# Performance work log

Measured on AMD Instinct MI355X. Metric: run time of the kernel, lower is better.

The kernel has to match this reference:

```python
import jax, jax.numpy as jnp
import numpy as np

B, S, D = 4, 1024, 1024
H = 16
DH = D // H  # head dim = 64
SCALE = DH ** -0.5
NEG = -1e18


def setup_inputs() -> dict:
    key = jax.random.key(0)
    ks = jax.random.split(key, 8)
    queries = jax.random.normal(ks[0], (B, S, D), dtype=jnp.float32)
    keys_ = jax.random.normal(ks[1], (B, S, D), dtype=jnp.float32)
    values = jax.random.normal(ks[2], (B, S, D), dtype=jnp.float32)
    mask = jax.random.randint(ks[3], (B, 1, S), 0, 2).astype(bool)
    sd = 1.0 / np.sqrt(D)
    Wq = jax.random.normal(ks[4], (D, D), dtype=jnp.float32) * sd
    Wk = jax.random.normal(ks[5], (D, D), dtype=jnp.float32) * sd
    Wv = jax.random.normal(ks[6], (D, D), dtype=jnp.float32) * sd
    Wo = jax.random.normal(ks[7], (D, D), dtype=jnp.float32) * sd
    return {"queries": queries, "keys": keys_, "values": values,
            "Wq": Wq, "Wk": Wk, "Wv": Wv, "Wo": Wo, "mask": mask}


def _split_heads(x):
    # [B,S,D] -> [B,H,S,DH]
    b, s, d = x.shape
    return x.reshape(b, s, H, d // H).transpose(0, 2, 1, 3)


def reference(queries, keys, values, Wq, Wk, Wv, Wo, mask):
    q = _split_heads(queries @ Wq) * SCALE          # [B,H,S,DH]
    k = _split_heads(keys @ Wk)                     # [B,H,S,DH]
    v = _split_heads(values @ Wv)                   # [B,H,S,DH]
    logits = jnp.einsum('bhqd,bhkd->bhqk', q, k)    # [B,H,S,S]
    # mask [B,1,Lk] -> unsqueeze head dim -> broadcast over [B,H,Lq,Lk]
    logits = jnp.where(mask[:, None, :, :], NEG, logits)
    attention_weights = logits.sum(axis=1) / H      # [B,S,S] head-averaged logits
    w = jax.nn.softmax(logits, axis=-1)             # dropout p=0 -> identity
    ctx = jnp.einsum('bhqk,bhkd->bhqd', w, v)       # [B,H,S,DH]
    ctx = ctx.transpose(0, 2, 1, 3).reshape(q.shape[0], q.shape[2], H * DH)
    outputs = ctx @ Wo                              # [B,S,D]
    return (outputs, attention_weights)
```

## Files before the change

kernel.cpp:

```cpp
#include <hip/hip_runtime.h>
#include <hip/hip_bf16.h>

typedef __bf16 bf16;
typedef __attribute__((ext_vector_type(8))) __bf16 bf16x8;
typedef __attribute__((ext_vector_type(4))) __bf16 bf16x4;
typedef __attribute__((ext_vector_type(4))) float f32x4;

#define NEGV (-1e18f)
#define LOG2E 1.4426950408889634f

__device__ __forceinline__ bf16 f2b(float f) {
    unsigned u = __builtin_bit_cast(unsigned, f);
    u += 0x7fffu + ((u >> 16) & 1u);
    unsigned short h = (unsigned short)(u >> 16);
    return __builtin_bit_cast(bf16, h);
}

__device__ __forceinline__ f32x4 mfma16(bf16x8 a, bf16x8 b, f32x4 c) {
    return __builtin_amdgcn_mfma_f32_16x16x32_bf16(a, b, c, 0, 0, 0);
}

__device__ __forceinline__ void gl16(const void* g, void* l) {
    __builtin_amdgcn_global_load_lds((const __attribute__((address_space(1))) void*)g,
                                     (__attribute__((address_space(3))) void*)l, 16, 0, 0);
}

__global__ __launch_bounds__(256) void prep(const float* __restrict__ Qf,
                                            const float* __restrict__ Kf,
                                            const float* __restrict__ Vf,
                                            const float* __restrict__ W0,
                                            const float* __restrict__ W1,
                                            const float* __restrict__ W2,
                                            const float* __restrict__ W3,
                                            bf16* __restrict__ Qa,
                                            bf16* __restrict__ Ka,
                                            bf16* __restrict__ Va,
                                            bf16* __restrict__ Wout) {
    __shared__ float tile[64][65];
    int bx = blockIdx.x;
    int t = threadIdx.x;
    if (bx < 6144) {
        int z = bx >> 11, x = bx & 2047;
        const float* in = (z == 0) ? Qf : (z == 1) ? Kf : Vf;
        bf16* out = (z == 0) ? Qa : (z == 1) ? Ka : Va;
        size_t i = ((size_t)x * 256 + t) * 8;
        float4 a = *(const float4*)&in[i];
        float4 b = *(const float4*)&in[i + 4];
        bf16x8 o;
        o[0] = f2b(a.x); o[1] = f2b(a.y); o[2] = f2b(a.z); o[3] = f2b(a.w);
        o[4] = f2b(b.x); o[5] = f2b(b.y); o[6] = f2b(b.z); o[7] = f2b(b.w);
        *(bf16x8*)&out[i] = o;
        return;
    }
    int w = bx - 6144;
    int z = w >> 8;
    const float* Ws[4] = {W0, W1, W2, W3};
    const float* W = Ws[z];
    bf16* O = Wout + ((size_t)z << 20);
    int k0 = (w & 15) * 64, n0 = ((w >> 4) & 15) * 64;
#pragma unroll
    for (int p = 0; p < 4; p++) {
        int r = (t >> 4) + p * 16, c = (t & 15) * 4;
        float4 v = *(const float4*)&W[(size_t)(k0 + r) * 1024 + n0 + c];
        tile[r][c] = v.x; tile[r][c + 1] = v.y; tile[r][c + 2] = v.z; tile[r][c + 3] = v.w;
    }
    __syncthreads();
#pragma unroll
    for (int p = 0; p < 4; p++) {
        int r = (t >> 4) + p * 16, c = (t & 15) * 4;
        bf16x4 o;
        o[0] = f2b(tile[c][r]); o[1] = f2b(tile[c + 1][r]);
        o[2] = f2b(tile[c + 2][r]); o[3] = f2b(tile[c + 3][r]);
        *(bf16x4*)&O[(size_t)(n0 + r) * 1024 + k0 + c] = o;
    }
}

__global__ __launch_bounds__(512, 1) void gemm8(const bf16* __restrict__ Qa,
                                                const bf16* __restrict__ Ka,
                                                const bf16* __restrict__ Va,
                                                const bf16* __restrict__ WtQ,
                                                bf16* __restrict__ Qw,
                                                bf16* __restrict__ Kw,
                                                bf16* __restrict__ VtG) {
    __shared__ bf16 LA[2][256 * 64];
    __shared__ bf16 LB[2][256 * 64];
    char* LAB = (char*)LA;
    char* LBB = (char*)LB;
    int t = threadIdx.x;
    int z = blockIdx.z;
    const bf16* A = (z == 0) ? Qa : (z == 1) ? Ka : Va;
    const bf16* Bt = WtQ + ((size_t)z << 20);
    int m0 = blockIdx.x * 256, n0 = blockIdx.y * 256;
    int wid = t >> 6, lane = t & 63;
    int wr = wid >> 2, wc = wid & 3, lr = lane & 15, lg = lane >> 4;
    const int sxl = (lr & 7) << 4;
    const int arow = wr * 128 + lr;
    const int brow = wc * 64 + lr;
    const int c0 = t, c1 = t + 512;
    const int r0 = c0 >> 3, q0 = (c0 & 7) ^ (r0 & 7);
    const int r1 = c1 >> 3, q1 = (c1 & 7) ^ (r1 & 7);

    f32x4 zero = {0.f, 0.f, 0.f, 0.f};
    f32x4 acc[8][4];
#pragma unroll
    for (int m = 0; m < 8; m++)
#pragma unroll
        for (int n = 0; n < 4; n++) acc[m][n] = zero;
    bf16x8 a[4][2], b0[2][2], b1[2][2];

#define STG_A(BUF, HALF, KT)                                                   \
    gl16(&A[(size_t)(m0 + (HALF) * 128 + r0) * 1024 + (KT) * 64 + q0 * 8],     \
         (void*)(LAB + (BUF) * 32768 + (HALF) * 16384 + c0 * 16));             \
    gl16(&A[(size_t)(m0 + (HALF) * 128 + r1) * 1024 + (KT) * 64 + q1 * 8],     \
         (void*)(LAB + (BUF) * 32768 + (HALF) * 16384 + c1 * 16));
#define STG_B(BUF, HALF, KT)                                                   \
    gl16(&Bt[(size_t)(n0 + (HALF) * 128 + r0) * 1024 + (KT) * 64 + q0 * 8],    \
         (void*)(LBB + (BUF) * 32768 + (HALF) * 16384 + c0 * 16));             \
    gl16(&Bt[(size_t)(n0 + (HALF) * 128 + r1) * 1024 + (KT) * 64 + q1 * 8],    \
         (void*)(LBB + (BUF) * 32768 + (HALF) * 16384 + c1 * 16));
#define STG_A2(BUF, KT) STG_A(BUF, 0, KT); STG_A(BUF, 1, KT);
#define STG_B2(BUF, KT) STG_B(BUF, 0, KT); STG_B(BUF, 1, KT);
#define RD_A(BUF, MH)                                                          \
    {                                                                          \
        _Pragma("unroll") for (int m = 0; m < 4; m++) {                        \
            int row = arow + (MH) * 64 + m * 16;                               \
            _Pragma("unroll") for (int ks = 0; ks < 2; ks++)                   \
                a[m][ks] = *(const bf16x8*)(LAB + (BUF) * 32768 +              \
                           ((row * 128 + ks * 64 + lg * 16) ^ sxl));           \
        }                                                                      \
    }
#define RD_B(BUF, NH, DST)                                                     \
    {                                                                          \
        _Pragma("unroll") for (int n = 0; n < 2; n++) {                        \
            int row = brow + (NH) * 32 + n * 16;                               \
            _Pragma("unroll") for (int ks = 0; ks < 2; ks++)                   \
                DST[n][ks] = *(const bf16x8*)(LBB + (BUF) * 32768 +            \
                             ((row * 128 + ks * 64 + lg * 16) ^ sxl));         \
        }                                                                      \
    }
#define MM(MH, NH, BB)                                                         \
    {                                                                          \
        _Pragma("unroll") for (int m = 0; m < 4; m++)                          \
        _Pragma("unroll") for (int n = 0; n < 2; n++)                          \
        _Pragma("unroll") for (int ks = 0; ks < 2; ks++)                       \
            acc[(MH) * 4 + m][(NH) * 2 + n] =                                  \
                mfma16(a[m][ks], BB[n][ks], acc[(MH) * 4 + m][(NH) * 2 + n]);  \
    }
#define PH_PRE                                                                 \
    __builtin_amdgcn_s_barrier();                                              \
    asm volatile("s_waitcnt lgkmcnt(0)" ::: "memory");                         \
    __builtin_amdgcn_sched_barrier(0);                                         \
    __builtin_amdgcn_s_setprio(1);
#define PH_POST                                                                \
    __builtin_amdgcn_s_setprio(0);                                             \
    __builtin_amdgcn_s_barrier();
#define VM4_BAR                                                                \
    __builtin_amdgcn_s_setprio(0);                                             \
    asm volatile("s_waitcnt vmcnt(4)" ::: "memory");                           \
    __builtin_amdgcn_s_barrier();

    STG_A2(0, 0); STG_B2(0, 0);
    STG_B2(1, 1);
    asm volatile("s_waitcnt vmcnt(4)" ::: "memory");
    __builtin_amdgcn_s_barrier();

    for (int i = 0; i < 7; i++) {
        int kt = 2 * i;
        RD_A(0, 0); RD_B(0, 0, b0); RD_B(0, 1, b1); STG_A2(1, kt + 1);
        PH_PRE; MM(0, 0, b0); MM(0, 1, b1); PH_POST;
        RD_A(0, 1); STG_B2(0, kt + 2);
        PH_PRE; MM(1, 0, b0); MM(1, 1, b1); VM4_BAR;
        RD_A(1, 0); RD_B(1, 0, b0); RD_B(1, 1, b1); STG_A2(0, kt + 2);
        PH_PRE; MM(0, 0, b0); MM(0, 1, b1); PH_POST;
        RD_A(1, 1); STG_B2(1, kt + 3);
        PH_PRE; MM(1, 0, b0); MM(1, 1, b1); VM4_BAR;
    }
    RD_A(0, 0); RD_B(0, 0, b0); RD_B(0, 1, b1); STG_A2(1, 15);
    PH_PRE; MM(0, 0, b0); MM(0, 1, b1); PH_POST;
    RD_A(0, 1);
    PH_PRE; MM(1, 0, b0); MM(1, 1, b1);
    __builtin_amdgcn_s_setprio(0);
    asm volatile("s_waitcnt vmcnt(0)" ::: "memory");
    __builtin_amdgcn_s_barrier();
    RD_A(1, 0); RD_B(1, 0, b0); RD_B(1, 1, b1);
    PH_PRE; MM(0, 0, b0); MM(0, 1, b1); PH_POST;
    RD_A(1, 1);
    PH_PRE; MM(1, 0, b0); MM(1, 1, b1);
    __builtin_amdgcn_s_setprio(0);
#undef STG_A
#undef STG_B
#undef STG_A2
#undef STG_B2
#undef RD_A
#undef RD_B
#undef MM
#undef PH_PRE
#undef PH_POST
#undef VM4_BAR
#pragma unroll
    for (int m = 0; m < 8; m++) {
        int rowg = m0 + wr * 128 + m * 16 + lg * 4;
#pragma unroll
        for (int n = 0; n < 4; n++) {
            int colg = n0 + wc * 64 + n * 16 + lr;
            if (z == 2) {
                bf16x4 o;
#pragma unroll
                for (int j = 0; j < 4; j++) o[j] = f2b(acc[m][n][j]);
                *(bf16x4*)&VtG[(size_t)colg * 4096 + rowg] = o;
            } else {
                bf16* C = (z == 0) ? Qw : Kw;
                float sc = (z == 0) ? 0.125f : 1.0f;
#pragma unroll
                for (int j = 0; j < 4; j++)
                    C[(size_t)(rowg + j) * 1024 + colg] = f2b(acc[m][n][j] * sc);
            }
        }
    }
}

__global__ __launch_bounds__(256, 3) void gemm_oa(const bf16* __restrict__ CTX,
                                                  const bf16* __restrict__ WtO,
                                                  float* __restrict__ out,
                                                  const bf16* __restrict__ Qw,
                                                  const bf16* __restrict__ Kw,
                                                  float* __restrict__ aw,
                                                  const int* __restrict__ maskp) {
    __shared__ bf16 As[128 * 64];
    __shared__ bf16 Bs[128 * 64];
    char* AsB = (char*)As;
    char* BsB = (char*)Bs;
    int t = threadIdx.x;
    int z = blockIdx.z;
    int bx = blockIdx.x;
    int m0, n0 = blockIdx.y * 128;
    const bf16* A;
    const bf16* Bt;
    float* C;
    const int* mask = nullptr;
    if (z == 0) {
        m0 = bx * 128;
        A = CTX; Bt = WtO; C = out;
    } else {
        int b = bx >> 3;
        m0 = (bx & 7) * 128;
        A = Qw + ((size_t)b << 20); Bt = Kw + ((size_t)b << 20);
        C = aw + ((size_t)b << 20); mask = maskp + b * 1024;
    }
    int wid = t >> 6, lane = t & 63;
    int wr = wid >> 1, wc = wid & 1, lr = lane & 15, lg = lane >> 4;
    f32x4 zero = {0.f, 0.f, 0.f, 0.f};
    f32x4 acc[4][4];
#pragma unroll
    for (int m = 0; m < 4; m++)
#pragma unroll
        for (int n = 0; n < 4; n++) acc[m][n] = zero;

    for (int k0 = 0; k0 < 1024; k0 += 64) {
        __syncthreads();
#pragma unroll
        for (int i = 0; i < 4; i++) {
            int c = wid * 256 + i * 64 + lane;
            int row = c >> 3, q = (c & 7) ^ (row & 7);
            gl16(&A[(size_t)(m0 + row) * 1024 + k0 + q * 8], (void*)&As[c * 8]);
            gl16(&Bt[(size_t)(n0 + row) * 1024 + k0 + q * 8], (void*)&Bs[c * 8]);
        }
        __syncthreads();
#pragma unroll
        for (int kk = 0; kk < 2; kk++) {
            bf16x8 af[4], bfr[4];
#pragma unroll
            for (int m = 0; m < 4; m++) {
                int row = wr * 64 + m * 16 + lr;
                af[m] = *(const bf16x8*)(AsB + ((row * 128 + kk * 64 + lg * 16) ^ ((row & 7) << 4)));
            }
#pragma unroll
            for (int n = 0; n < 4; n++) {
                int row = wc * 64 + n * 16 + lr;
                bfr[n] = *(const bf16x8*)(BsB + ((row * 128 + kk * 64 + lg * 16) ^ ((row & 7) << 4)));
            }
#pragma unroll
            for (int m = 0; m < 4; m++)
#pragma unroll
                for (int n = 0; n < 4; n++) acc[m][n] = mfma16(af[m], bfr[n], acc[m][n]);
        }
    }
#pragma unroll
    for (int n = 0; n < 4; n++) {
        int colg = n0 + wc * 64 + n * 16 + lr;
        int mk = (z == 1) ? mask[colg] : 0;
#pragma unroll
        for (int m = 0; m < 4; m++) {
            int rowg = m0 + wr * 64 + m * 16 + lg * 4;
#pragma unroll
            for (int j = 0; j < 4; j++) {
                float v = acc[m][n][j];
                size_t idx = (size_t)(rowg + j) * 1024 + colg;
                if (z == 0) C[idx] = v;
                else C[idx] = mk ? NEGV : v * (1.f / 16.f);
            }
        }
    }
}

__global__ __launch_bounds__(256, 4) void flash_k(const bf16* __restrict__ Q,
                                                  const bf16* __restrict__ K,
                                                  const bf16* __restrict__ VT,
                                                  bf16* __restrict__ CTX,
                                                  const int* __restrict__ maskp) {
    __shared__ bf16 Ks[2][64 * 64];
    __shared__ bf16 Vs[64 * 64];
    __shared__ bf16 Ps[4][16 * 64];
    __shared__ float biasS[1024];
    int raw = blockIdx.x;
    int idx = raw >> 3;
    int bh = (raw & 7) * 8 + (idx & 7);
    int qt = idx >> 3;
    int b = bh >> 4, h = bh & 15;
    int t = threadIdx.x, wid = t >> 6, lane = t & 63;
    int lr = lane & 15, lg = lane >> 4;
    int qbase = qt * 64 + wid * 16;
    const size_t bS = (size_t)b * 1024;
    char* KsB = (char*)Ks;
    char* VsB = (char*)Vs;
    char* PsW = (char*)&Ps[wid][0];
    const int sxl = (lr & 7) << 4;

    {
        int4 mv = *(const int4*)&maskp[b * 1024 + t * 4];
        float4 bv;
        const float NB = NEGV * LOG2E;
        bv.x = mv.x ? NB : 0.f; bv.y = mv.y ? NB : 0.f;
        bv.z = mv.z ? NB : 0.f; bv.w = mv.w ? NB : 0.f;
        *(float4*)&biasS[t * 4] = bv;
    }

    bf16x8 qf[2];
#pragma unroll
    for (int c = 0; c < 2; c++)
        qf[c] = *(const bf16x8*)&Q[(bS + qbase + lr) * 1024 + h * 64 + c * 32 + lg * 8];

    f32x4 zero = {0.f, 0.f, 0.f, 0.f};
    f32x4 acc[4];
#pragma unroll
    for (int d = 0; d < 4; d++) acc[d] = zero;
    float lsum = 0.f;

    const bf16* Kbase = K + bS * 1024 + h * 64;
    const bf16* Vbase = VT + (size_t)(h * 64) * 4096 + bS;

    int c0 = t, c1 = t + 256;
    int kr0 = c0 >> 3, kq0 = c0 & 7, kr1 = c1 >> 3, kq1 = c1 & 7;
    const int kw0 = (kr0 * 128 + kq0 * 16) ^ ((kr0 & 7) << 4);
    const int kw1 = (kr1 * 128 + kq1 * 16) ^ ((kr1 & 7) << 4);

    {
        bf16x8 t0 = *(const bf16x8*)&Kbase[(size_t)kr0 * 1024 + kq0 * 8];
        bf16x8 t1 = *(const bf16x8*)&Kbase[(size_t)kr1 * 1024 + kq1 * 8];
        *(bf16x8*)(KsB + kw0) = t0;
        *(bf16x8*)(KsB + kw1) = t1;
    }
    bf16x8 kg[2], vg[2];
    vg[0] = *(const bf16x8*)&Vbase[(size_t)kr0 * 4096 + kq0 * 8];
    vg[1] = *(const bf16x8*)&Vbase[(size_t)kr1 * 4096 + kq1 * 8];
    kg[0] = *(const bf16x8*)&Kbase[(size_t)(64 + kr0) * 1024 + kq0 * 8];
    kg[1] = *(const bf16x8*)&Kbase[(size_t)(64 + kr1) * 1024 + kq1 * 8];

    int cur = 0;
    for (int kt = 0; kt < 16; kt++) {
        __syncthreads();
        *(bf16x8*)(VsB + kw0) = vg[0];
        *(bf16x8*)(VsB + kw1) = vg[1];
        if (kt < 15) {
            *(bf16x8*)(KsB + (cur ^ 1) * 8192 + kw0) = kg[0];
            *(bf16x8*)(KsB + (cur ^ 1) * 8192 + kw1) = kg[1];
            size_t ko = (size_t)(kt + 1) * 64;
            vg[0] = *(const bf16x8*)&Vbase[(size_t)kr0 * 4096 + ko + kq0 * 8];
            vg[1] = *(const bf16x8*)&Vbase[(size_t)kr1 * 4096 + ko + kq1 * 8];
            if (kt < 14) {
                kg[0] = *(const bf16x8*)&Kbase[(ko + 64 + kr0) * 1024 + kq0 * 8];
                kg[1] = *(const bf16x8*)&Kbase[(ko + 64 + kr1) * 1024 + kq1 * 8];
            }
        }
        f32x4 s[4];
        __builtin_amdgcn_s_setprio(1);
#pragma unroll
        for (int n = 0; n < 4; n++) {
            int row = n * 16 + lr;
            bf16x8 kf0 = *(const bf16x8*)(KsB + cur * 8192 + ((row * 128 + lg * 16) ^ sxl));
            bf16x8 kf1 = *(const bf16x8*)(KsB + cur * 8192 + ((row * 128 + 64 + lg * 16) ^ sxl));
            f32x4 zz = zero;
            zz = mfma16(kf0, qf[0], zz);
            zz = mfma16(kf1, qf[1], zz);
            s[n] = zz;
        }
        __builtin_amdgcn_s_setprio(0);
        __syncthreads();
        float r0 = 0.f, r1 = 0.f, r2 = 0.f, r3 = 0.f;
#pragma unroll
        for (int n = 0; n < 4; n++) {
            float4 bv = *(const float4*)&biasS[kt * 64 + n * 16 + lg * 4];
            float p0 = __builtin_exp2f(__builtin_fmaf(s[n][0], LOG2E, bv.x));
            float p1 = __builtin_exp2f(__builtin_fmaf(s[n][1], LOG2E, bv.y));
            float p2 = __builtin_exp2f(__builtin_fmaf(s[n][2], LOG2E, bv.z));
            float p3 = __builtin_exp2f(__builtin_fmaf(s[n][3], LOG2E, bv.w));
            r0 += p0; r1 += p1; r2 += p2; r3 += p3;
            bf16x4 o;
            o[0] = (bf16)p0; o[1] = (bf16)p1; o[2] = (bf16)p2; o[3] = (bf16)p3;
            *(bf16x4*)(PsW + ((lr * 128 + n * 32 + lg * 8) ^ sxl)) = o;
        }
        lsum += (r0 + r1) + (r2 + r3);
        __builtin_amdgcn_s_setprio(1);
#pragma unroll
        for (int c = 0; c < 2; c++) {
            bf16x8 pa = *(const bf16x8*)(PsW + ((lr * 128 + c * 64 + lg * 16) ^ sxl));
#pragma unroll
            for (int d = 0; d < 4; d++) {
                int row = d * 16 + lr;
                bf16x8 vb = *(const bf16x8*)(VsB + ((row * 128 + c * 64 + lg * 16) ^ ((row & 7) << 4)));
                acc[d] = mfma16(pa, vb, acc[d]);
            }
        }
        __builtin_amdgcn_s_setprio(0);
        cur ^= 1;
    }
    lsum += __shfl_xor(lsum, 16);
    lsum += __shfl_xor(lsum, 32);
    float lb[4];
#pragma unroll
    for (int j = 0; j < 4; j++) lb[j] = __shfl(lsum, lg * 4 + j);
#pragma unroll
    for (int j = 0; j < 4; j++) {
        float inv = 1.f / lb[j];
#pragma unroll
        for (int d = 0; d < 4; d++)
            CTX[(bS + qbase + lg * 4 + j) * 1024 + h * 64 + d * 16 + lr] = f2b(acc[d][j] * inv);
    }
}

extern "C" void kernel_launch(void* const* d_in, const int* in_sizes, int n_in,
                              void* d_out, int out_size, void* d_ws, size_t ws_size,
                              hipStream_t stream) {
    const float* queries = (const float*)d_in[0];
    const float* keys    = (const float*)d_in[1];
    const float* values  = (const float*)d_in[2];
    const float* Wq = (const float*)d_in[3];
    const float* Wk = (const float*)d_in[4];
    const float* Wv = (const float*)d_in[5];
    const float* Wo = (const float*)d_in[6];
    const int* mask = (const int*)d_in[7];

    float* out = (float*)d_out;
    float* aw  = out + ((size_t)4 << 20);

    bf16* wsb = (bf16*)d_ws;
    bf16* WtQ = wsb;
    bf16* Qa  = wsb + ((size_t)4 << 20);
    bf16* Qw  = wsb + ((size_t)8 << 20);
    bf16* Kw  = wsb + ((size_t)12 << 20);
    bf16* VtG = wsb + ((size_t)16 << 20);
    bf16* Ka  = (bf16*)aw;
    bf16* Va  = (bf16*)aw + ((size_t)4 << 20);
    bf16* CTX = Qa;

    prep<<<dim3(7168), 256, 0, stream>>>(queries, keys, values, Wq, Wk, Wv, Wo,
                                         Qa, Ka, Va, WtQ);
    gemm8<<<dim3(16, 4, 3), 512, 0, stream>>>(Qa, Ka, Va, WtQ, Qw, Kw, VtG);
    flash_k<<<dim3(1024), 256, 0, stream>>>(Qw, Kw, VtG, CTX, mask);
    gemm_oa<<<dim3(32, 8, 2), 256, 0, stream>>>(CTX, WtQ + ((size_t)3 << 20), out,
                                                Qw, Kw, aw, mask);
}
```

Measured before the change: 116.7 us.

## Fuse fp32-to-bf16 activation conversion into projection GEMM A-tile loads

Drops the separate conversion pass that turned the fp32 Q/K/V activations into bf16 buffers. The projection GEMM now loads fp32 A tiles into registers, converts them, and writes them swizzled into LDS, with a register double-buffered prefetch two k-tiles ahead and reworked vmcnt gating. This removes a full read and write of the activations plus part of the prep launch. In exchange the GEMM reads twice the A bytes, uses more registers, and relies on fragile hand-tuned waitcnt counts.

```diff
diff --git a/kernel.cpp b/kernel.cpp
--- a/kernel.cpp
+++ b/kernel.cpp
@@ -25,34 +25,14 @@
                                      (__attribute__((address_space(3))) void*)l, 16, 0, 0);
 }
 
-__global__ __launch_bounds__(256) void prep(const float* __restrict__ Qf,
-                                            const float* __restrict__ Kf,
-                                            const float* __restrict__ Vf,
-                                            const float* __restrict__ W0,
+__global__ __launch_bounds__(256) void prep(const float* __restrict__ W0,
                                             const float* __restrict__ W1,
                                             const float* __restrict__ W2,
                                             const float* __restrict__ W3,
-                                            bf16* __restrict__ Qa,
-                                            bf16* __restrict__ Ka,
-                                            bf16* __restrict__ Va,
                                             bf16* __restrict__ Wout) {
     __shared__ float tile[64][65];
-    int bx = blockIdx.x;
+    int w = blockIdx.x;
     int t = threadIdx.x;
-    if (bx < 6144) {
-        int z = bx >> 11, x = bx & 2047;
-        const float* in = (z == 0) ? Qf : (z == 1) ? Kf : Vf;
-        bf16* out = (z == 0) ? Qa : (z == 1) ? Ka : Va;
-        size_t i = ((size_t)x * 256 + t) * 8;
-        float4 a = *(const float4*)&in[i];
-        float4 b = *(const float4*)&in[i + 4];
-        bf16x8 o;
-        o[0] = f2b(a.x); o[1] = f2b(a.y); o[2] = f2b(a.z); o[3] = f2b(a.w);
-        o[4] = f2b(b.x); o[5] = f2b(b.y); o[6] = f2b(b.z); o[7] = f2b(b.w);
-        *(bf16x8*)&out[i] = o;
-        return;
-    }
-    int w = bx - 6144;
     int z = w >> 8;
     const float* Ws[4] = {W0, W1, W2, W3};
     const float* W = Ws[z];
@@ -75,9 +55,9 @@
     }
 }
 
-__global__ __launch_bounds__(512, 1) void gemm8(const bf16* __restrict__ Qa,
-                                                const bf16* __restrict__ Ka,
-                                                const bf16* __restrict__ Va,
+__global__ __launch_bounds__(512, 1) void gemm8(const float* __restrict__ Qf,
+                                                const float* __restrict__ Kf,
+                                                const float* __restrict__ Vf,
                                                 const bf16* __restrict__ WtQ,
                                                 bf16* __restrict__ Qw,
                                                 bf16* __restrict__ Kw,
@@ -88,7 +68,7 @@
     char* LBB = (char*)LB;
     int t = threadIdx.x;
     int z = blockIdx.z;
-    const bf16* A = (z == 0) ? Qa : (z == 1) ? Ka : Va;
+    const float* A = (z == 0) ? Qf : (z == 1) ? Kf : Vf;
     const bf16* Bt = WtQ + ((size_t)z << 20);
     int m0 = blockIdx.x * 256, n0 = blockIdx.y * 256;
     int wid = t >> 6, lane = t & 63;
@@ -99,6 +79,16 @@
     const int c0 = t, c1 = t + 512;
     const int r0 = c0 >> 3, q0 = (c0 & 7) ^ (r0 & 7);
     const int r1 = c1 >> 3, q1 = (c1 & 7) ^ (r1 & 7);
+    int arw[4], aq[4], ahalf[4], alof[4];
+#pragma unroll
+    for (int j = 0; j < 4; j++) {
+        int c = t + j * 512;
+        int row = c >> 3, q = c & 7;
+        arw[j] = row; aq[j] = q;
+        ahalf[j] = row >> 7;
+        int lrow = row & 127;
+        alof[j] = (ahalf[j] << 14) + (((lrow * 128 + q * 16)) ^ ((lrow & 7) << 4));
+    }
 
     f32x4 zero = {0.f, 0.f, 0.f, 0.f};
     f32x4 acc[8][4];
@@ -107,19 +97,36 @@
 #pragma unroll
         for (int n = 0; n < 4; n++) acc[m][n] = zero;
     bf16x8 a[4][2], b0[2][2], b1[2][2];
-
-#define STG_A(BUF, HALF, KT)                                                   \
-    gl16(&A[(size_t)(m0 + (HALF) * 128 + r0) * 1024 + (KT) * 64 + q0 * 8],     \
-         (void*)(LAB + (BUF) * 32768 + (HALF) * 16384 + c0 * 16));             \
-    gl16(&A[(size_t)(m0 + (HALF) * 128 + r1) * 1024 + (KT) * 64 + q1 * 8],     \
-         (void*)(LAB + (BUF) * 32768 + (HALF) * 16384 + c1 * 16));
-#define STG_B(BUF, HALF, KT)                                                   \
-    gl16(&Bt[(size_t)(n0 + (HALF) * 128 + r0) * 1024 + (KT) * 64 + q0 * 8],    \
-         (void*)(LBB + (BUF) * 32768 + (HALF) * 16384 + c0 * 16));             \
-    gl16(&Bt[(size_t)(n0 + (HALF) * 128 + r1) * 1024 + (KT) * 64 + q1 * 8],    \
-         (void*)(LBB + (BUF) * 32768 + (HALF) * 16384 + c1 * 16));
-#define STG_A2(BUF, KT) STG_A(BUF, 0, KT); STG_A(BUF, 1, KT);
-#define STG_B2(BUF, KT) STG_B(BUF, 0, KT); STG_B(BUF, 1, KT);
+    float4 S1[4][2], S2[4][2];
+
+#define LOADF(SET, KT)                                                         \
+    {                                                                          \
+        _Pragma("unroll") for (int j = 0; j < 4; j++) {                        \
+            const float* src = &A[(size_t)(m0 + arw[j]) * 1024 + (KT) * 64 + aq[j] * 8]; \
+            SET[j][0] = *(const float4*)src;                                   \
+            SET[j][1] = *(const float4*)(src + 4);                             \
+        }                                                                      \
+    }
+#define DSW_A(BUF, SET)                                                        \
+    {                                                                          \
+        _Pragma("unroll") for (int j = 0; j < 4; j++) {                        \
+            bf16x8 o;                                                          \
+            o[0] = f2b(SET[j][0].x); o[1] = f2b(SET[j][0].y);                  \
+            o[2] = f2b(SET[j][0].z); o[3] = f2b(SET[j][0].w);                  \
+            o[4] = f2b(SET[j][1].x); o[5] = f2b(SET[j][1].y);                  \
+            o[6] = f2b(SET[j][1].z); o[7] = f2b(SET[j][1].w);                  \
+            *(bf16x8*)(LAB + (BUF) * 32768 + alof[j]) = o;                     \
+        }                                                                      \
+    }
+#define STG_B2(BUF, KT)                                                        \
+    gl16(&Bt[(size_t)(n0 + r0) * 1024 + (KT) * 64 + q0 * 8],                   \
+         (void*)(LBB + (BUF) * 32768 + c0 * 16));                              \
+    gl16(&Bt[(size_t)(n0 + r1) * 1024 + (KT) * 64 + q1 * 8],                   \
+         (void*)(LBB + (BUF) * 32768 + c1 * 16));                              \
+    gl16(&Bt[(size_t)(n0 + 128 + r0) * 1024 + (KT) * 64 + q0 * 8],             \
+         (void*)(LBB + (BUF) * 32768 + 16384 + c0 * 16));                      \
+    gl16(&Bt[(size_t)(n0 + 128 + r1) * 1024 + (KT) * 64 + q1 * 8],             \
+         (void*)(LBB + (BUF) * 32768 + 16384 + c1 * 16));
 #define RD_A(BUF, MH)                                                          \
     {                                                                          \
         _Pragma("unroll") for (int m = 0; m < 4; m++) {                        \
@@ -154,28 +161,44 @@
 #define PH_POST                                                                \
     __builtin_amdgcn_s_setprio(0);                                             \
     __builtin_amdgcn_s_barrier();
-#define VM4_BAR                                                                \
+#define GATE12                                                                 \
     __builtin_amdgcn_s_setprio(0);                                             \
-    asm volatile("s_waitcnt vmcnt(4)" ::: "memory");                           \
+    asm volatile("s_waitcnt vmcnt(12)" ::: "memory");                          \
     __builtin_amdgcn_s_barrier();
 
-    STG_A2(0, 0); STG_B2(0, 0);
+    LOADF(S1, 0);
+    STG_B2(0, 0);
     STG_B2(1, 1);
-    asm volatile("s_waitcnt vmcnt(4)" ::: "memory");
+    asm volatile("s_waitcnt vmcnt(8)" ::: "memory");
+    DSW_A(0, S1);
+    LOADF(S1, 1);
+    LOADF(S2, 2);
+    asm volatile("s_waitcnt vmcnt(16)" ::: "memory");
+    asm volatile("s_waitcnt lgkmcnt(0)" ::: "memory");
     __builtin_amdgcn_s_barrier();
+    asm volatile("s_waitcnt vmcnt(8)" ::: "memory");
 
     for (int i = 0; i < 7; i++) {
         int kt = 2 * i;
-        RD_A(0, 0); RD_B(0, 0, b0); RD_B(0, 1, b1); STG_A2(1, kt + 1);
+        int kt3 = (kt + 3 < 15) ? kt + 3 : 15;
+        int kt4 = (kt + 4 < 15) ? kt + 4 : 15;
+        RD_A(0, 0); RD_B(0, 0, b0); RD_B(0, 1, b1);
+        DSW_A(1, S1);
+        LOADF(S1, kt3);
         PH_PRE; MM(0, 0, b0); MM(0, 1, b1); PH_POST;
-        RD_A(0, 1); STG_B2(0, kt + 2);
-        PH_PRE; MM(1, 0, b0); MM(1, 1, b1); VM4_BAR;
-        RD_A(1, 0); RD_B(1, 0, b0); RD_B(1, 1, b1); STG_A2(0, kt + 2);
+        RD_A(0, 1);
+        STG_B2(0, kt + 2);
+        PH_PRE; MM(1, 0, b0); MM(1, 1, b1); GATE12;
+        RD_A(1, 0); RD_B(1, 0, b0); RD_B(1, 1, b1);
+        DSW_A(0, S2);
+        LOADF(S2, kt4);
         PH_PRE; MM(0, 0, b0); MM(0, 1, b1); PH_POST;
-        RD_A(1, 1); STG_B2(1, kt + 3);
-        PH_PRE; MM(1, 0, b0); MM(1, 1, b1); VM4_BAR;
-    }
-    RD_A(0, 0); RD_B(0, 0, b0); RD_B(0, 1, b1); STG_A2(1, 15);
+        RD_A(1, 1);
+        STG_B2(1, kt + 3);
+        PH_PRE; MM(1, 0, b0); MM(1, 1, b1); GATE12;
+    }
+    RD_A(0, 0); RD_B(0, 0, b0); RD_B(0, 1, b1);
+    DSW_A(1, S1);
     PH_PRE; MM(0, 0, b0); MM(0, 1, b1); PH_POST;
     RD_A(0, 1);
     PH_PRE; MM(1, 0, b0); MM(1, 1, b1);
@@ -187,16 +210,15 @@
     RD_A(1, 1);
     PH_PRE; MM(1, 0, b0); MM(1, 1, b1);
     __builtin_amdgcn_s_setprio(0);
-#undef STG_A
-#undef STG_B
-#undef STG_A2
+#undef LOADF
+#undef DSW_A
 #undef STG_B2
 #undef RD_A
 #undef RD_B
 #undef MM
 #undef PH_PRE
 #undef PH_POST
-#undef VM4_BAR
+#undef GATE12
 #pragma unroll
     for (int m = 0; m < 8; m++) {
         int rowg = m0 + wr * 128 + m * 16 + lg * 4;
@@ -455,17 +477,13 @@
 
     bf16* wsb = (bf16*)d_ws;
     bf16* WtQ = wsb;
-    bf16* Qa  = wsb + ((size_t)4 << 20);
+    bf16* CTX = wsb + ((size_t)4 << 20);
     bf16* Qw  = wsb + ((size_t)8 << 20);
     bf16* Kw  = wsb + ((size_t)12 << 20);
     bf16* VtG = wsb + ((size_t)16 << 20);
-    bf16* Ka  = (bf16*)aw;
-    bf16* Va  = (bf16*)aw + ((size_t)4 << 20);
-    bf16* CTX = Qa;
-
-    prep<<<dim3(7168), 256, 0, stream>>>(queries, keys, values, Wq, Wk, Wv, Wo,
-                                         Qa, Ka, Va, WtQ);
-    gemm8<<<dim3(16, 4, 3), 512, 0, stream>>>(Qa, Ka, Va, WtQ, Qw, Kw, VtG);
+
+    prep<<<dim3(1024), 256, 0, stream>>>(Wq, Wk, Wv, Wo, WtQ);
+    gemm8<<<dim3(16, 4, 3), 512, 0, stream>>>(queries, keys, values, WtQ, Qw, Kw, VtG);
     flash_k<<<dim3(1024), 256, 0, stream>>>(Qw, Kw, VtG, CTX, mask);
     gemm_oa<<<dim3(32, 8, 2), 256, 0, stream>>>(CTX, WtQ + ((size_t)3 << 20), out,
                                                 Qw, Kw, aw, mask);
```

Result: slower. 222.7 us (+90.8%).

## Replace 256x256 pipelined QKV projection GEMM with simpler 128x128 tile kernel

Applied to the files above, without the earlier changes.

Replaces the hand-pipelined 256x256-tile, 512-thread, double-buffered QKV projection GEMM with a single-buffered 128x128-tile, 256-thread kernel that allows up to three blocks per CU. The grid grows from 192 to 768 blocks, which should fill the CUs better and let occupancy hide load latency instead of explicit software pipelining. In exchange it gives up the prefetch/compute overlap and priority scheduling, and each tile reuses loaded data less, so global traffic rises.

```diff
diff --git a/kernel.cpp b/kernel.cpp
--- a/kernel.cpp
+++ b/kernel.cpp
@@ -75,134 +75,66 @@
     }
 }
 
-__global__ __launch_bounds__(512, 1) void gemm8(const bf16* __restrict__ Qa,
-                                                const bf16* __restrict__ Ka,
-                                                const bf16* __restrict__ Va,
-                                                const bf16* __restrict__ WtQ,
-                                                bf16* __restrict__ Qw,
-                                                bf16* __restrict__ Kw,
-                                                bf16* __restrict__ VtG) {
-    __shared__ bf16 LA[2][256 * 64];
-    __shared__ bf16 LB[2][256 * 64];
-    char* LAB = (char*)LA;
-    char* LBB = (char*)LB;
+__global__ __launch_bounds__(256, 3) void gemm_proj3(const bf16* __restrict__ Qa,
+                                                     const bf16* __restrict__ Ka,
+                                                     const bf16* __restrict__ Va,
+                                                     const bf16* __restrict__ WtQ,
+                                                     bf16* __restrict__ Qw,
+                                                     bf16* __restrict__ Kw,
+                                                     bf16* __restrict__ VtG) {
+    __shared__ bf16 As[128 * 64];
+    __shared__ bf16 Bs[128 * 64];
+    char* AsB = (char*)As;
+    char* BsB = (char*)Bs;
     int t = threadIdx.x;
     int z = blockIdx.z;
     const bf16* A = (z == 0) ? Qa : (z == 1) ? Ka : Va;
     const bf16* Bt = WtQ + ((size_t)z << 20);
-    int m0 = blockIdx.x * 256, n0 = blockIdx.y * 256;
+    int m0 = blockIdx.x * 128, n0 = blockIdx.y * 128;
     int wid = t >> 6, lane = t & 63;
-    int wr = wid >> 2, wc = wid & 3, lr = lane & 15, lg = lane >> 4;
-    const int sxl = (lr & 7) << 4;
-    const int arow = wr * 128 + lr;
-    const int brow = wc * 64 + lr;
-    const int c0 = t, c1 = t + 512;
-    const int r0 = c0 >> 3, q0 = (c0 & 7) ^ (r0 & 7);
-    const int r1 = c1 >> 3, q1 = (c1 & 7) ^ (r1 & 7);
-
+    int wr = wid >> 1, wc = wid & 1, lr = lane & 15, lg = lane >> 4;
     f32x4 zero = {0.f, 0.f, 0.f, 0.f};
-    f32x4 acc[8][4];
-#pragma unroll
-    for (int m = 0; m < 8; m++)
+    f32x4 acc[4][4];
+#pragma unroll
+    for (int m = 0; m < 4; m++)
 #pragma unroll
         for (int n = 0; n < 4; n++) acc[m][n] = zero;
-    bf16x8 a[4][2], b0[2][2], b1[2][2];
-
-#define STG_A(BUF, HALF, KT)                                                   \
-    gl16(&A[(size_t)(m0 + (HALF) * 128 + r0) * 1024 + (KT) * 64 + q0 * 8],     \
-         (void*)(LAB + (BUF) * 32768 + (HALF) * 16384 + c0 * 16));             \
-    gl16(&A[(size_t)(m0 + (HALF) * 128 + r1) * 1024 + (KT) * 64 + q1 * 8],     \
-         (void*)(LAB + (BUF) * 32768 + (HALF) * 16384 + c1 * 16));
-#define STG_B(BUF, HALF, KT)                                                   \
-    gl16(&Bt[(size_t)(n0 + (HALF) * 128 + r0) * 1024 + (KT) * 64 + q0 * 8],    \
-         (void*)(LBB + (BUF) * 32768 + (HALF) * 16384 + c0 * 16));             \
-    gl16(&Bt[(size_t)(n0 + (HALF) * 128 + r1) * 1024 + (KT) * 64 + q1 * 8],    \
-         (void*)(LBB + (BUF) * 32768 + (HALF) * 16384 + c1 * 16));
-#define STG_A2(BUF, KT) STG_A(BUF, 0, KT); STG_A(BUF, 1, KT);
-#define STG_B2(BUF, KT) STG_B(BUF, 0, KT); STG_B(BUF, 1, KT);
-#define RD_A(BUF, MH)                                                          \
-    {                                                                          \
-        _Pragma("unroll") for (int m = 0; m < 4; m++) {                        \
-            int row = arow + (MH) * 64 + m * 16;                               \
-            _Pragma("unroll") for (int ks = 0; ks < 2; ks++)                   \
-                a[m][ks] = *(const bf16x8*)(LAB + (BUF) * 32768 +              \
-                           ((row * 128 + ks * 64 + lg * 16) ^ sxl));           \
-        }                                                                      \
-    }
-#define RD_B(BUF, NH, DST)                                                     \
-    {                                                                          \
-        _Pragma("unroll") for (int n = 0; n < 2; n++) {                        \
-            int row = brow + (NH) * 32 + n * 16;                               \
-            _Pragma("unroll") for (int ks = 0; ks < 2; ks++)                   \
-                DST[n][ks] = *(const bf16x8*)(LBB + (BUF) * 32768 +            \
-                             ((row * 128 + ks * 64 + lg * 16) ^ sxl));         \
-        }                                                                      \
-    }
-#define MM(MH, NH, BB)                                                         \
-    {                                                                          \
-        _Pragma("unroll") for (int m = 0; m < 4; m++)                          \
-        _Pragma("unroll") for (int n = 0; n < 2; n++)                          \
-        _Pragma("unroll") for (int ks = 0; ks < 2; ks++)                       \
-            acc[(MH) * 4 + m][(NH) * 2 + n] =                                  \
-                mfma16(a[m][ks], BB[n][ks], acc[(MH) * 4 + m][(NH) * 2 + n]);  \
-    }
-#define PH_PRE                                                                 \
-    __builtin_amdgcn_s_barrier();                                              \
-    asm volatile("s_waitcnt lgkmcnt(0)" ::: "memory");                         \
-    __builtin_amdgcn_sched_barrier(0);                                         \
-    __builtin_amdgcn_s_setprio(1);
-#define PH_POST                                                                \
-    __builtin_amdgcn_s_setprio(0);                                             \
-    __builtin_amdgcn_s_barrier();
-#define VM4_BAR                                                                \
-    __builtin_amdgcn_s_setprio(0);                                             \
-    asm volatile("s_waitcnt vmcnt(4)" ::: "memory");                           \
-    __builtin_amdgcn_s_barrier();
-
-    STG_A2(0, 0); STG_B2(0, 0);
-    STG_B2(1, 1);
-    asm volatile("s_waitcnt vmcnt(4)" ::: "memory");
-    __builtin_amdgcn_s_barrier();
-
-    for (int i = 0; i < 7; i++) {
-        int kt = 2 * i;
-        RD_A(0, 0); RD_B(0, 0, b0); RD_B(0, 1, b1); STG_A2(1, kt + 1);
-        PH_PRE; MM(0, 0, b0); MM(0, 1, b1); PH_POST;
-        RD_A(0, 1); STG_B2(0, kt + 2);
-        PH_PRE; MM(1, 0, b0); MM(1, 1, b1); VM4_BAR;
-        RD_A(1, 0); RD_B(1, 0, b0); RD_B(1, 1, b1); STG_A2(0, kt + 2);
-        PH_PRE; MM(0, 0, b0); MM(0, 1, b1); PH_POST;
-        RD_A(1, 1); STG_B2(1, kt + 3);
-        PH_PRE; MM(1, 0, b0); MM(1, 1, b1); VM4_BAR;
-    }
-    RD_A(0, 0); RD_B(0, 0, b0); RD_B(0, 1, b1); STG_A2(1, 15);
-    PH_PRE; MM(0, 0, b0); MM(0, 1, b1); PH_POST;
-    RD_A(0, 1);
-    PH_PRE; MM(1, 0, b0); MM(1, 1, b1);
-    __builtin_amdgcn_s_setprio(0);
-    asm volatile("s_waitcnt vmcnt(0)" ::: "memory");
-    __builtin_amdgcn_s_barrier();
-    RD_A(1, 0); RD_B(1, 0, b0); RD_B(1, 1, b1);
-    PH_PRE; MM(0, 0, b0); MM(0, 1, b1); PH_POST;
-    RD_A(1, 1);
-    PH_PRE; MM(1, 0, b0); MM(1, 1, b1);
-    __builtin_amdgcn_s_setprio(0);
-#undef STG_A
-#undef STG_B
-#undef STG_A2
-#undef STG_B2
-#undef RD_A
-#undef RD_B
-#undef MM
-#undef PH_PRE
-#undef PH_POST
-#undef VM4_BAR
-#pragma unroll
-    for (int m = 0; m < 8; m++) {
-        int rowg = m0 + wr * 128 + m * 16 + lg * 4;
-#pragma unroll
-        for (int n = 0; n < 4; n++) {
-            int colg = n0 + wc * 64 + n * 16 + lr;
+
+    for (int k0 = 0; k0 < 1024; k0 += 64) {
+        __syncthreads();
+#pragma unroll
+        for (int i = 0; i < 4; i++) {
+            int c = wid * 256 + i * 64 + lane;
+            int row = c >> 3, q = (c & 7) ^ (row & 7);
+            gl16(&A[(size_t)(m0 + row) * 1024 + k0 + q * 8], (void*)&As[c * 8]);
+            gl16(&Bt[(size_t)(n0 + row) * 1024 + k0 + q * 8], (void*)&Bs[c * 8]);
+        }
+        __syncthreads();
+#pragma unroll
+        for (int kk = 0; kk < 2; kk++) {
+            bf16x8 af[4], bfr[4];
+#pragma unroll
+            for (int m = 0; m < 4; m++) {
+                int row = wr * 64 + m * 16 + lr;
+                af[m] = *(const bf16x8*)(AsB + ((row * 128 + kk * 64 + lg * 16) ^ ((row & 7) << 4)));
+            }
+#pragma unroll
+            for (int n = 0; n < 4; n++) {
+                int row = wc * 64 + n * 16 + lr;
+                bfr[n] = *(const bf16x8*)(BsB + ((row * 128 + kk * 64 + lg * 16) ^ ((row & 7) << 4)));
+            }
+#pragma unroll
+            for (int m = 0; m < 4; m++)
+#pragma unroll
+                for (int n = 0; n < 4; n++) acc[m][n] = mfma16(af[m], bfr[n], acc[m][n]);
+        }
+    }
+#pragma unroll
+    for (int n = 0; n < 4; n++) {
+        int colg = n0 + wc * 64 + n * 16 + lr;
+#pragma unroll
+        for (int m = 0; m < 4; m++) {
+            int rowg = m0 + wr * 64 + m * 16 + lg * 4;
             if (z == 2) {
                 bf16x4 o;
 #pragma unroll
@@ -465,7 +397,7 @@
 
     prep<<<dim3(7168), 256, 0, stream>>>(queries, keys, values, Wq, Wk, Wv, Wo,
                                          Qa, Ka, Va, WtQ);
-    gemm8<<<dim3(16, 4, 3), 512, 0, stream>>>(Qa, Ka, Va, WtQ, Qw, Kw, VtG);
+    gemm_proj3<<<dim3(32, 8, 3), 256, 0, stream>>>(Qa, Ka, Va, WtQ, Qw, Kw, VtG);
     flash_k<<<dim3(1024), 256, 0, stream>>>(Qw, Kw, VtG, CTX, mask);
     gemm_oa<<<dim3(32, 8, 2), 256, 0, stream>>>(CTX, WtQ + ((size_t)3 << 20), out,
                                                 Qw, Kw, aw, mask);
```

Measured after the change: 109.7 us, median of 2. 1.06x faster.
